# Kernel optimization log

Hardware: AMD Instinct MI355X
Metric: run time of the kernel (lower is better)

## Reference

```python
import jax, jax.numpy as jnp
import numpy as np

E, H2, V = 128, 512, 50000  # embedding_size, hidden_size*2, output_size
H4 = 2 * H2


def _gru_cell(x, h, W_ih, W_hh, b_ih, b_hh):
    # PyTorch GRU cell: gates ordered (r, z, n)
    gi = x @ W_ih.T + b_ih
    gh = h @ W_hh.T + b_hh
    i_r, i_z, i_n = jnp.split(gi, 3, axis=-1)
    h_r, h_z, h_n = jnp.split(gh, 3, axis=-1)
    r = jax.nn.sigmoid(i_r + h_r)
    z = jax.nn.sigmoid(i_z + h_z)
    n = jnp.tanh(i_n + r * h_n)
    return (1.0 - z) * n + z * h


def setup_inputs() -> dict:
    key = jax.random.key(0)
    ks = jax.random.split(key, 24)
    B, T = 64, 400
    s = 0.02
    inp = {
        "input_ids": jax.random.randint(ks[0], (B, 1), 0, V),
        "pre_hidden": jax.random.normal(ks[1], (2, B, H2), jnp.float32),
        "encoder_outputs": jax.random.normal(ks[2], (B, T, H2), jnp.float32),
        "source_input": jax.random.randint(ks[3], (B, T), 0, V),
        "coverage_vector": jax.random.uniform(ks[4], (B, 1, T), jnp.float32),
        "emb_table": jax.random.normal(ks[5], (V, E), jnp.float32) * s,
        "W_ih0": jax.random.normal(ks[6], (3 * H2, E), jnp.float32) * s,
        "W_hh0": jax.random.normal(ks[7], (3 * H2, H2), jnp.float32) * s,
        "b_ih0": jnp.zeros((3 * H2,), jnp.float32),
        "b_hh0": jnp.zeros((3 * H2,), jnp.float32),
        "W_ih1": jax.random.normal(ks[8], (3 * H2, H2), jnp.float32) * s,
        "W_hh1": jax.random.normal(ks[9], (3 * H2, H2), jnp.float32) * s,
        "b_ih1": jnp.zeros((3 * H2,), jnp.float32),
        "b_hh1": jnp.zeros((3 * H2,), jnp.float32),
        "align_W": jax.random.normal(ks[10], (1, 3 * H2), jnp.float32) * s,
        "align_b": jnp.zeros((1,), jnp.float32),
        "cov_W": jax.random.normal(ks[11], (H2, 1), jnp.float32) * s,
        "cov_b": jnp.zeros((H2,), jnp.float32),
        "fc1_W": jax.random.normal(ks[12], (H4, H4), jnp.float32) * s,
        "fc1_b": jnp.zeros((H4,), jnp.float32),
        "fc2_W": jax.random.normal(ks[13], (V, H4), jnp.float32) * s,
        "fc2_b": jnp.zeros((V,), jnp.float32),
        "gen_W": jax.random.normal(ks[14], (1, H4 + E), jnp.float32) * s,
        "gen_b": jnp.zeros((1,), jnp.float32),
    }
    return inp


def reference(input_ids, pre_hidden, encoder_outputs, source_input, coverage_vector,
              emb_table, W_ih0, W_hh0, b_ih0, b_hh0, W_ih1, W_hh1, b_ih1, b_hh1,
              align_W, align_b, cov_W, cov_b, fc1_W, fc1_b, fc2_W, fc2_b, gen_W, gen_b):
    B, T = source_input.shape
    # embedding lookup (dropout omitted / eval mode)
    emb = emb_table[input_ids[:, 0]]                          # [B,E]
    # 2-layer GRU, single decode step
    h0 = _gru_cell(emb, pre_hidden[0], W_ih0, W_hh0, b_ih0, b_hh0)
    h1 = _gru_cell(h0, pre_hidden[1], W_ih1, W_hh1, b_ih1, b_hh1)
    current_hidden = jnp.stack([h0, h1], axis=0)              # [2,B,H2]
    s = h1                                                    # [B,H2]
    cov = coverage_vector[:, 0, :]                            # [B,T]
    # coverage projection: Linear(1 -> H2)
    cov_feat = cov[:, :, None] * cov_W[:, 0][None, None, :] + cov_b  # [B,T,H2]
    s_rep = jnp.broadcast_to(s[:, None, :], (B, T, s.shape[-1]))
    combine = jnp.concatenate([encoder_outputs, s_rep, cov_feat], axis=-1)  # [B,T,3*H2]
    scores = jnp.einsum('bti,i->bt', combine, align_W[0]) + align_b[0]
    attn = jax.nn.softmax(jnp.tanh(scores), axis=1)           # [B,T]
    # coverage loss: sum of elementwise min(attn, coverage)
    coverage_loss = jnp.sum(jnp.minimum(attn, cov))
    new_coverage = coverage_vector + attn[:, None, :]         # [B,1,T]
    context = jnp.einsum('bt,bth->bh', attn, encoder_outputs) # [B,H2]
    ni = jnp.tanh(jnp.concatenate([s, context], axis=-1) @ fc1_W.T + fc1_b)
    logits = ni @ fc2_W.T + fc2_b                             # [B,V]
    Pvocab = jax.nn.softmax(logits, axis=1)
    # vectorized copy distribution: scatter-add attention mass onto source token ids
    batch_idx = jnp.arange(B)[:, None]
    copy_prob = jnp.zeros((B, logits.shape[1]), logits.dtype).at[batch_idx, source_input].add(attn)
    gen_in = jnp.concatenate([context, s, emb], axis=-1)      # [B,H4+E]
    p_gen = jax.nn.sigmoid(gen_in @ gen_W.T + gen_b)          # [B,1]
    out = Pvocab * p_gen + copy_prob * (1.0 - p_gen)
    return (out, current_hidden, attn[:, None, :], copy_prob, new_coverage, coverage_loss)
```

## Files before the change

### kernel.cpp

```cpp
#include <hip/hip_runtime.h>
#include <hip/hip_bf16.h>
#include <cstddef>

#define BB 64
#define TT 400
#define EE 128
#define HH 512
#define H4 1024
#define VV 50000
#define NCH 8
#define LSTR 136

#define OFF_OUT     0
#define OFF_CURHID  (BB*VV)
#define OFF_ATTN    (OFF_CURHID + 2*BB*HH)
#define OFF_COPY    (OFF_ATTN + BB*TT)
#define OFF_NEWCOV  (OFF_COPY + BB*VV)
#define OFF_LOSS    (OFF_NEWCOV + BB*TT)

#define WS_S      0
#define WS_ESC    (WS_S + BB*HH)
#define WS_ATTN   (WS_ESC + BB*TT)
#define WS_NIB    (WS_ATTN + BB*TT)
#define WS_A1     (WS_NIB + BB*H4/2)
#define WS_AX0    (WS_A1 + BB*H4/2)
#define WS_AH0    (WS_AX0 + BB*EE/2)
#define WS_AH1    (WS_AH0 + BB*HH/2)
#define WS_AX1    (WS_AH1 + BB*HH/2)
#define WS_PGEN   (WS_AX1 + BB*HH/2)
#define WS_RM     (WS_PGEN + 64)
#define WS_RS     (WS_RM + 64)
#define WS_CTXP   (WS_RS + 64)
#define WS_LOGITS (WS_CTXP + BB*NCH*HH)

typedef __attribute__((ext_vector_type(8))) short short8v;
typedef __attribute__((ext_vector_type(4))) short short4v;
typedef __attribute__((ext_vector_type(4))) float f32x4;

__device__ __forceinline__ float wredsum(float v) {
#pragma unroll
  for (int o = 32; o > 0; o >>= 1) v += __shfl_down(v, o, 64);
  return v;
}
__device__ __forceinline__ float wredmax(float v) {
#pragma unroll
  for (int o = 32; o > 0; o >>= 1) v = fmaxf(v, __shfl_down(v, o, 64));
  return v;
}
__device__ __forceinline__ float dot4(float4 a, float4 b) {
  return a.x*b.x + a.y*b.y + a.z*b.z + a.w*b.w;
}
__device__ __forceinline__ float sigmoidf(float x) { return 1.f / (1.f + expf(-x)); }
__device__ __forceinline__ short bfh(float f) {
  union { __hip_bfloat16 h; short s; } u; u.h = __float2bfloat16(f); return u.s;
}
__device__ __forceinline__ float bf2f(short s) {
  union { unsigned int u; float f; } v; v.u = ((unsigned int)(unsigned short)s) << 16; return v.f;
}

__global__ void zero_prep_kernel(float* __restrict__ p, float* __restrict__ loss,
                                 float* __restrict__ rs,
                                 const float* __restrict__ embt, const int* __restrict__ ids,
                                 const float* __restrict__ preh,
                                 const float* __restrict__ enc, const float* __restrict__ aW,
                                 short* __restrict__ ax0, short* __restrict__ ah0,
                                 short* __restrict__ ah1, float* __restrict__ esc) {
  int i = blockIdx.x * 256 + threadIdx.x;
  ((float4*)p)[i] = make_float4(0.f, 0.f, 0.f, 0.f);
  if (i == 0) loss[0] = 0.f;
  if (i < 64) rs[i] = 0.f;
  if (i < BB * EE) {
    int b = i >> 7, k = i & 127;
    ax0[i] = bfh(embt[(size_t)ids[b] * EE + k]);
  } else if (i < BB * EE + 2 * BB * HH) {
    int j = i - BB * EE;
    if (j < BB * HH) ah0[j] = bfh(preh[j]);
    else ah1[j - BB * HH] = bfh(preh[j]);
  }
  int wgid = blockIdx.x * 4 + (threadIdx.x >> 6);
  int lane = threadIdx.x & 63;
  int i8 = lane * 8;
  float4 a0 = *(const float4*)&aW[i8];
  float4 a1 = *(const float4*)&aW[i8 + 4];
  for (int idx = wgid; idx < BB * TT; idx += 12500) {
    const float* e = enc + (size_t)idx * HH + i8;
    float d = dot4(*(const float4*)&e[0], a0) + dot4(*(const float4*)&e[4], a1);
    d = wredsum(d);
    if (lane == 0) esc[idx] = d;
  }
}

template<int KX>
__global__ __launch_bounds__(768) void gru_mfma_kernel(
    const short* __restrict__ Ax, const short* __restrict__ Ah,
    const float* __restrict__ W_ih, const float* __restrict__ W_hh,
    const float* __restrict__ b_ih, const float* __restrict__ b_hh,
    const float* __restrict__ hprev,
    float* __restrict__ hout_f, float* __restrict__ hout_o,
    short* __restrict__ hout_b, int bstride) {
  __shared__ float Pf[12 * 256];
  const int w = threadIdx.x >> 6;
  const int lane = threadIdx.x & 63;
  const int r16 = lane & 15, kg = lane >> 4;
  const int j0 = (blockIdx.x & 31) * 16;
  const int bg = blockIdx.x >> 5;
  const int half = (w >= 6) ? 1 : 0;
  const int wv = w - half * 6;
  const int part = (wv >= 3) ? 1 : 0;
  const int g = wv - part * 3;
  const int K = part ? HH : KX;
  const int Kh = K >> 1;
  const float* Wm = part ? W_hh : W_ih;
  const short* Am = part ? Ah : Ax;

  f32x4 acc = {0.f, 0.f, 0.f, 0.f};
  const float* wp = Wm + (size_t)(g * HH + j0 + r16) * K + half * Kh + kg * 8;
  const short* ap = Am + (size_t)(bg * 16 + r16) * K + half * Kh + kg * 8;
#pragma unroll 4
  for (int k0 = 0; k0 < Kh; k0 += 32) {
    float4 w0 = *(const float4*)(wp + k0);
    float4 w1 = *(const float4*)(wp + k0 + 4);
    short8v a = *(const short8v*)(ap + k0);
    short8v bf;
    bf[0] = bfh(w0.x); bf[1] = bfh(w0.y); bf[2] = bfh(w0.z); bf[3] = bfh(w0.w);
    bf[4] = bfh(w1.x); bf[5] = bfh(w1.y); bf[6] = bfh(w1.z); bf[7] = bfh(w1.w);
    acc = __builtin_amdgcn_mfma_f32_16x16x32_bf16(a, bf, acc, 0, 0, 0);
  }
  float* pw = Pf + (half * 6 + part * 3 + g) * 256;
#pragma unroll
  for (int r = 0; r < 4; r++) pw[(kg * 4 + r) * 16 + r16] = acc[r];
  __syncthreads();
  if (w == 0) {
    int col = j0 + r16;
    float bir = b_ih[col] + b_hh[col];
    float biz = b_ih[HH + col] + b_hh[HH + col];
    float bin = b_ih[2 * HH + col], bhn = b_hh[2 * HH + col];
#pragma unroll
    for (int r = 0; r < 4; r++) {
      int m = kg * 4 + r;
      int row = bg * 16 + m;
      int o = m * 16 + r16;
      float ih_r = Pf[0 * 256 + o] + Pf[6 * 256 + o];
      float ih_z = Pf[1 * 256 + o] + Pf[7 * 256 + o];
      float ih_n = Pf[2 * 256 + o] + Pf[8 * 256 + o];
      float hh_r = Pf[3 * 256 + o] + Pf[9 * 256 + o];
      float hh_z = Pf[4 * 256 + o] + Pf[10 * 256 + o];
      float hh_n = Pf[5 * 256 + o] + Pf[11 * 256 + o];
      float rv = sigmoidf(ih_r + hh_r + bir);
      float zv = sigmoidf(ih_z + hh_z + biz);
      float nv = tanhf(ih_n + bin + rv * (hh_n + bhn));
      float h = (1.f - zv) * nv + zv * hprev[(size_t)row * HH + col];
      hout_f[(size_t)row * HH + col] = h;
      hout_o[(size_t)row * HH + col] = h;
      hout_b[(size_t)row * bstride + col] = bfh(h);
    }
  }
}

__global__ void attn_kernel(const float* __restrict__ esc, const float* __restrict__ cov,
                            const int* __restrict__ src, const float* __restrict__ s,
                            const float* __restrict__ aW, const float* __restrict__ ab,
                            const float* __restrict__ covW, const float* __restrict__ covb,
                            float* __restrict__ wattn, float* __restrict__ dout,
                            float* __restrict__ outc) {
  int b = blockIdx.x, tid = threadIdx.x;
  int lane = tid & 63, wid = tid >> 6;
  __shared__ float sred[24];
  __shared__ float bval[8];
  {
    float a2 = aW[2 * HH + tid];
    float p1 = s[(size_t)b * HH + tid] * aW[HH + tid];
    float p2 = covW[tid] * a2;
    float p3 = covb[tid] * a2;
    float r1 = wredsum(p1), r2 = wredsum(p2), r3 = wredsum(p3);
    if (lane == 0) { sred[wid] = r1; sred[8 + wid] = r2; sred[16 + wid] = r3; }
    __syncthreads();
    if (wid == 0) {
      float q1 = (lane < 8) ? sred[lane] : 0.f;      q1 = wredsum(q1);
      float q2 = (lane < 8) ? sred[8 + lane] : 0.f;  q2 = wredsum(q2);
      float q3 = (lane < 8) ? sred[16 + lane] : 0.f; q3 = wredsum(q3);
      if (lane == 0) { bval[2] = q1; bval[3] = q2; bval[4] = q3 + ab[0]; }
    }
    __syncthreads();
  }
  float sdot = bval[2], c1 = bval[3], c0 = bval[4];
  float cvt = (tid < TT) ? cov[b * TT + tid] : 0.f;
  float v = (tid < TT) ? tanhf(esc[b * TT + tid] + sdot + cvt * c1 + c0) : -1e30f;
  float wm = wredmax(v);
  if (lane == 0) sred[wid] = wm;
  __syncthreads();
  if (wid == 0) {
    float r = (lane < 8) ? sred[lane] : -1e30f;
    r = wredmax(r);
    if (lane == 0) bval[0] = r;
  }
  __syncthreads();
  float m = bval[0];
  float e = (tid < TT) ? expf(v - m) : 0.f;
  float wsm = wredsum(e);
  __syncthreads();
  if (lane == 0) sred[wid] = wsm;
  __syncthreads();
  if (wid == 0) {
    float r = (lane < 8) ? sred[lane] : 0.f;
    r = wredsum(r);
    if (lane == 0) bval[1] = r;
  }
  __syncthreads();
  float denom = bval[1];
  float a = e / denom;
  float lp = 0.f;
  if (tid < TT) {
    wattn[b * TT + tid] = a;
    dout[OFF_ATTN + b * TT + tid] = a;
    dout[OFF_NEWCOV + b * TT + tid] = cvt + a;
    lp = fminf(a, cvt);
    atomicAdd(&outc[(size_t)b * VV + src[b * TT + tid]], a);
  }
  float wl = wredsum(lp);
  __syncthreads();
  if (lane == 0) sred[wid] = wl;
  __syncthreads();
  if (wid == 0) {
    float r = (lane < 8) ? sred[lane] : 0.f;
    r = wredsum(r);
    if (lane == 0) atomicAdd(&dout[OFF_LOSS], r);
  }
}

__global__ void ctx_part_kernel(const float* __restrict__ enc, const float* __restrict__ attn,
                                float* __restrict__ ctxp) {
  int b = blockIdx.x, c = blockIdx.y;
  int h = threadIdx.x;
  __shared__ float as[TT / NCH];
  if (h < TT / NCH) as[h] = attn[b * TT + c * (TT / NCH) + h];
  __syncthreads();
  const float* e = enc + ((size_t)b * TT + c * (TT / NCH)) * HH + h;
  float acc = 0.f;
#pragma unroll 10
  for (int t = 0; t < TT / NCH; t++) acc += as[t] * e[(size_t)t * HH];
  ctxp[((size_t)b * NCH + c) * HH + h] = acc;
}

__global__ void ctxred_pgen_kernel(const float* __restrict__ ctxp, const float* __restrict__ s,
                                   const float* __restrict__ embt, const int* __restrict__ ids,
                                   const float* __restrict__ gW, const float* __restrict__ gb,
                                   short* __restrict__ a1, float* __restrict__ pgen) {
  int b = blockIdx.x, tid = threadIdx.x;
  int lane = tid & 63, wid = tid >> 6;
  __shared__ float sred[8];
  float acc = 0.f;
#pragma unroll
  for (int c = 0; c < NCH; c++) acc += ctxp[((size_t)b * NCH + c) * HH + tid];
  a1[(size_t)b * H4 + HH + tid] = bfh(acc);
  float part = acc * gW[tid] + s[b * HH + tid] * gW[HH + tid];
  if (tid < EE) part += embt[(size_t)ids[b] * EE + tid] * gW[2 * HH + tid];
  float w = wredsum(part);
  if (lane == 0) sred[wid] = w;
  __syncthreads();
  if (wid == 0) {
    float r = (lane < 8) ? sred[lane] : 0.f;
    r = wredsum(r);
    if (lane == 0) pgen[b] = sigmoidf(r + gb[0]);
  }
}

__global__ __launch_bounds__(256) void fc1_kernel(const short* __restrict__ a1,
                                                  const float* __restrict__ W,
                                                  const float* __restrict__ bias,
                                                  short* __restrict__ nib) {
  __shared__ float part[4096];
  const int w = threadIdx.x >> 6;
  const int lane = threadIdx.x & 63;
  const int r16 = lane & 15, kg = lane >> 4;
  const int v0 = blockIdx.x * 16;
  const int kb = w * 256;

  f32x4 acc0 = {0.f,0.f,0.f,0.f}, acc1 = {0.f,0.f,0.f,0.f};
  f32x4 acc2 = {0.f,0.f,0.f,0.f}, acc3 = {0.f,0.f,0.f,0.f};
  const float* wp = W + (size_t)(v0 + r16) * H4 + kb + kg * 8;
  const short* ap = a1 + (size_t)r16 * H4 + kb + kg * 8;
#pragma unroll 4
  for (int k0 = 0; k0 < 256; k0 += 32) {
    float4 w0 = *(const float4*)(wp + k0);
    float4 w1 = *(const float4*)(wp + k0 + 4);
    short8v a0 = *(const short8v*)(ap + k0);
    short8v a1v = *(const short8v*)(ap + 16 * H4 + k0);
    short8v a2 = *(const short8v*)(ap + 32 * H4 + k0);
    short8v a3 = *(const short8v*)(ap + 48 * H4 + k0);
    short8v bf;
    bf[0] = bfh(w0.x); bf[1] = bfh(w0.y); bf[2] = bfh(w0.z); bf[3] = bfh(w0.w);
    bf[4] = bfh(w1.x); bf[5] = bfh(w1.y); bf[6] = bfh(w1.z); bf[7] = bfh(w1.w);
    acc0 = __builtin_amdgcn_mfma_f32_16x16x32_bf16(a0, bf, acc0, 0, 0, 0);
    acc1 = __builtin_amdgcn_mfma_f32_16x16x32_bf16(a1v, bf, acc1, 0, 0, 0);
    acc2 = __builtin_amdgcn_mfma_f32_16x16x32_bf16(a2, bf, acc2, 0, 0, 0);
    acc3 = __builtin_amdgcn_mfma_f32_16x16x32_bf16(a3, bf, acc3, 0, 0, 0);
  }
  float* pb = part + w * 1024;
#pragma unroll
  for (int r = 0; r < 4; r++) {
    pb[(kg * 4 + r) * 16 + r16]      = acc0[r];
    pb[(16 + kg * 4 + r) * 16 + r16] = acc1[r];
    pb[(32 + kg * 4 + r) * 16 + r16] = acc2[r];
    pb[(48 + kg * 4 + r) * 16 + r16] = acc3[r];
  }
  __syncthreads();
  int idx = threadIdx.x * 4;
  int m = idx >> 4, c0 = idx & 15;
  f32x4 s0 = *(const f32x4*)(part + idx);
  f32x4 s1 = *(const f32x4*)(part + 1024 + idx);
  f32x4 s2 = *(const f32x4*)(part + 2048 + idx);
  f32x4 s3 = *(const f32x4*)(part + 3072 + idx);
  f32x4 bv = *(const f32x4*)(bias + v0 + c0);
  f32x4 o = s0 + s1 + s2 + s3 + bv;
#pragma unroll
  for (int j = 0; j < 4; j++)
    nib[(size_t)m * H4 + v0 + c0 + j] = bfh(tanhf(o[j]));
}

__global__ __launch_bounds__(256) void fc2_kernel(const short* __restrict__ nib,
                                                  const float* __restrict__ W,
                                                  const float* __restrict__ bias,
                                                  short* __restrict__ logits_bf,
                                                  float* __restrict__ rs) {
  __shared__ short Wl[64 * LSTR];
  __shared__ short Al[64 * LSTR];
  const int tid = threadIdx.x;
  const int w = tid >> 6, lane = tid & 63;
  const int r16 = lane & 15, kg = lane >> 4;
  const int v0 = blockIdx.x * 64;
  const int srow = tid >> 2, quad = tid & 3;
  const int vr = min(v0 + srow, VV - 1);

  f32x4 acc[4];
#pragma unroll
  for (int i = 0; i < 4; i++) acc[i] = (f32x4){0.f, 0.f, 0.f, 0.f};

  const float* wsrc = W + (size_t)vr * H4 + quad * 4;
  const short* asrc = nib + (size_t)srow * H4 + quad * 8;

  float4 wregA[8], wregB[8];
  short8v areg[4];
#pragma unroll
  for (int j = 0; j < 8; j++) wregA[j] = *(const float4*)(wsrc + j * 16);
#pragma unroll
  for (int j = 0; j < 8; j++) wregB[j] = *(const float4*)(wsrc + 128 + j * 16);
#pragma unroll
  for (int j = 0; j < 4; j++) areg[j] = *(const short8v*)(asrc + j * 32);

  auto step = [&](float4 (&wcur)[8], int ks) {
    char* dst = (char*)Wl + srow * (LSTR * 2) + quad * 8;
#pragma unroll
    for (int j = 0; j < 8; j++) {
      float4 f = wcur[j];
      short4v h; h[0] = bfh(f.x); h[1] = bfh(f.y); h[2] = bfh(f.z); h[3] = bfh(f.w);
      *(short4v*)(dst + j * 32) = h;
    }
    char* adst = (char*)Al + srow * (LSTR * 2) + quad * 16;
#pragma unroll
    for (int j = 0; j < 4; j++)
      *(short8v*)(adst + j * 64) = areg[j];
    __syncthreads();
    if (ks < 6) {
#pragma unroll
      for (int j = 0; j < 8; j++) wcur[j] = *(const float4*)(wsrc + (ks + 2) * 128 + j * 16);
    }
    if (ks < 7) {
#pragma unroll
      for (int j = 0; j < 4; j++) areg[j] = *(const short8v*)(asrc + (ks + 1) * 128 + j * 32);
    }
#pragma unroll
    for (int s = 0; s < 4; s++) {
      short8v wf = *(const short8v*)((char*)Wl + (w * 16 + r16) * (LSTR * 2) + s * 64 + kg * 16);
#pragma unroll
      for (int i = 0; i < 4; i++) {
        short8v af = *(const short8v*)((char*)Al + (i * 16 + r16) * (LSTR * 2) + s * 64 + kg * 16);
        acc[i] = __builtin_amdgcn_mfma_f32_16x16x32_bf16(af, wf, acc[i], 0, 0, 0);
      }
    }
    __syncthreads();
  };
#pragma unroll
  for (int it = 0; it < 4; it++) {
    step(wregA, 2 * it);
    step(wregB, 2 * it + 1);
  }

  float* sc = (float*)Wl;
#pragma unroll
  for (int i = 0; i < 4; i++)
#pragma unroll
    for (int r = 0; r < 4; r++)
      sc[(i * 16 + kg * 4 + r) * 64 + w * 16 + r16] = acc[i][r];
  __syncthreads();
  int m = tid >> 2, q = tid & 3;
  int colbase = v0 + q * 16;
  float esum = 0.f;
  if (colbase < VV) {
    const float* scp = sc + m * 64 + q * 16;
    short8v lo, hi;
#pragma unroll
    for (int j = 0; j < 8; j++) {
      short lb = bfh(scp[j] + bias[colbase + j]);
      lo[j] = lb;
      esum += expf(bf2f(lb));
    }
#pragma unroll
    for (int j = 0; j < 8; j++) {
      short lb = bfh(scp[8 + j] + bias[colbase + 8 + j]);
      hi[j] = lb;
      esum += expf(bf2f(lb));
    }
    *(short8v*)(logits_bf + (size_t)m * VV + colbase)     = lo;
    *(short8v*)(logits_bf + (size_t)m * VV + colbase + 8) = hi;
  }
  esum += __shfl_down(esum, 2, 4);
  esum += __shfl_down(esum, 1, 4);
  if (q == 0) atomicAdd(&rs[m], esum);
}

__global__ void final_kernel(const short* __restrict__ logits_bf, const float* __restrict__ rs,
                             const float* __restrict__ pgen,
                             const float* __restrict__ copy, float* __restrict__ out) {
  int i = blockIdx.x * 256 + threadIdx.x;
  int b = (i * 4) / VV;
  float p = pgen[b], s = rs[b];
  short4v l = ((const short4v*)logits_bf)[i];
  float4 c = ((const float4*)copy)[i];
  float q = 1.f - p;
  float ps = p / s;
  float4 o;
  o.x = expf(bf2f(l[0])) * ps + c.x * q;
  o.y = expf(bf2f(l[1])) * ps + c.y * q;
  o.z = expf(bf2f(l[2])) * ps + c.z * q;
  o.w = expf(bf2f(l[3])) * ps + c.w * q;
  ((float4*)out)[i] = o;
}

extern "C" void kernel_launch(void* const* d_in, const int* in_sizes, int n_in,
                              void* d_out, int out_size, void* d_ws, size_t ws_size,
                              hipStream_t stream) {
  const int*   ids  = (const int*)d_in[0];
  const float* preh = (const float*)d_in[1];
  const float* enc  = (const float*)d_in[2];
  const int*   src  = (const int*)d_in[3];
  const float* cov  = (const float*)d_in[4];
  const float* embt = (const float*)d_in[5];
  const float* Wih0 = (const float*)d_in[6];
  const float* Whh0 = (const float*)d_in[7];
  const float* bih0 = (const float*)d_in[8];
  const float* bhh0 = (const float*)d_in[9];
  const float* Wih1 = (const float*)d_in[10];
  const float* Whh1 = (const float*)d_in[11];
  const float* bih1 = (const float*)d_in[12];
  const float* bhh1 = (const float*)d_in[13];
  const float* aW   = (const float*)d_in[14];
  const float* ab   = (const float*)d_in[15];
  const float* covW = (const float*)d_in[16];
  const float* covb = (const float*)d_in[17];
  const float* f1W  = (const float*)d_in[18];
  const float* f1b  = (const float*)d_in[19];
  const float* f2W  = (const float*)d_in[20];
  const float* f2b  = (const float*)d_in[21];
  const float* gW   = (const float*)d_in[22];
  const float* gb   = (const float*)d_in[23];
  float* out = (float*)d_out;
  float* ws  = (float*)d_ws;

  zero_prep_kernel<<<3125, 256, 0, stream>>>(out + OFF_COPY, out + OFF_LOSS, ws + WS_RS,
                                             embt, ids, preh, enc, aW,
                                             (short*)(ws + WS_AX0), (short*)(ws + WS_AH0),
                                             (short*)(ws + WS_AH1), ws + WS_ESC);
  gru_mfma_kernel<EE><<<128, 768, 0, stream>>>(
      (const short*)(ws + WS_AX0), (const short*)(ws + WS_AH0),
      Wih0, Whh0, bih0, bhh0, preh,
      out + OFF_CURHID, out + OFF_CURHID, (short*)(ws + WS_AX1), HH);
  gru_mfma_kernel<HH><<<128, 768, 0, stream>>>(
      (const short*)(ws + WS_AX1), (const short*)(ws + WS_AH1),
      Wih1, Whh1, bih1, bhh1, preh + BB * HH,
      ws + WS_S, out + OFF_CURHID + BB * HH, (short*)(ws + WS_A1), H4);
  attn_kernel<<<64, 512, 0, stream>>>(ws + WS_ESC, cov, src, ws + WS_S,
                                      aW, ab, covW, covb,
                                      ws + WS_ATTN, out, out + OFF_COPY);
  ctx_part_kernel<<<dim3(64, NCH), 512, 0, stream>>>(enc, ws + WS_ATTN, ws + WS_CTXP);
  ctxred_pgen_kernel<<<64, 512, 0, stream>>>(ws + WS_CTXP, ws + WS_S, embt, ids, gW, gb,
                                             (short*)(ws + WS_A1), ws + WS_PGEN);
  fc1_kernel<<<64, 256, 0, stream>>>((const short*)(ws + WS_A1), f1W, f1b,
                                     (short*)(ws + WS_NIB));
  fc2_kernel<<<782, 256, 0, stream>>>((const short*)(ws + WS_NIB), f2W, f2b,
                                      (short*)(ws + WS_LOGITS), ws + WS_RS);
  final_kernel<<<3125, 256, 0, stream>>>((const short*)(ws + WS_LOGITS), ws + WS_RS,
                                         ws + WS_PGEN, out + OFF_COPY, out);
}
```

Before: 122.4 us.

## Fuse attention softmax into context kernel and read fc2 activations from global

Merges the attention softmax kernel with the context partial-sum kernel. Each of the 8 chunk blocks per batch row recomputes the full softmax redundantly, and only chunk 0 writes the attention outputs, coverage, copy scatter and loss. This removes one launch and the workspace round-trip for the attention weights. Separately, fc2 no longer stages the bf16 activation tile in shared memory and loads MFMA A-fragments directly from global/L2 memory. That halves the LDS footprint but adds repeated global loads inside the inner loop.

```diff
diff --git a/kernel.cpp b/kernel.cpp
--- a/kernel.cpp
+++ b/kernel.cpp
@@ -9,6 +9,7 @@
 #define H4 1024
 #define VV 50000
 #define NCH 8
+#define TCH (TT/NCH)
 #define LSTR 136
 
 #define OFF_OUT     0
@@ -20,8 +21,7 @@
 
 #define WS_S      0
 #define WS_ESC    (WS_S + BB*HH)
-#define WS_ATTN   (WS_ESC + BB*TT)
-#define WS_NIB    (WS_ATTN + BB*TT)
+#define WS_NIB    (WS_ESC + BB*TT)
 #define WS_A1     (WS_NIB + BB*H4/2)
 #define WS_AX0    (WS_A1 + BB*H4/2)
 #define WS_AH0    (WS_AX0 + BB*EE/2)
@@ -157,14 +157,17 @@
   }
 }
 
-__global__ void attn_kernel(const float* __restrict__ esc, const float* __restrict__ cov,
-                            const int* __restrict__ src, const float* __restrict__ s,
-                            const float* __restrict__ aW, const float* __restrict__ ab,
-                            const float* __restrict__ covW, const float* __restrict__ covb,
-                            float* __restrict__ wattn, float* __restrict__ dout,
-                            float* __restrict__ outc) {
-  int b = blockIdx.x, tid = threadIdx.x;
+__global__ __launch_bounds__(512) void attn_ctx_kernel(
+    const float* __restrict__ esc, const float* __restrict__ cov,
+    const int* __restrict__ src, const float* __restrict__ s,
+    const float* __restrict__ aW, const float* __restrict__ ab,
+    const float* __restrict__ covW, const float* __restrict__ covb,
+    const float* __restrict__ enc,
+    float* __restrict__ dout, float* __restrict__ outc, float* __restrict__ ctxp) {
+  int b = blockIdx.x, c = blockIdx.y;
+  int tid = threadIdx.x;
   int lane = tid & 63, wid = tid >> 6;
+  __shared__ float as[TT];
   __shared__ float sred[24];
   __shared__ float bval[8];
   {
@@ -209,37 +212,32 @@
   __syncthreads();
   float denom = bval[1];
   float a = e / denom;
-  float lp = 0.f;
-  if (tid < TT) {
-    wattn[b * TT + tid] = a;
-    dout[OFF_ATTN + b * TT + tid] = a;
-    dout[OFF_NEWCOV + b * TT + tid] = cvt + a;
-    lp = fminf(a, cvt);
-    atomicAdd(&outc[(size_t)b * VV + src[b * TT + tid]], a);
-  }
-  float wl = wredsum(lp);
-  __syncthreads();
-  if (lane == 0) sred[wid] = wl;
-  __syncthreads();
-  if (wid == 0) {
-    float r = (lane < 8) ? sred[lane] : 0.f;
-    r = wredsum(r);
-    if (lane == 0) atomicAdd(&dout[OFF_LOSS], r);
-  }
-}
-
-__global__ void ctx_part_kernel(const float* __restrict__ enc, const float* __restrict__ attn,
-                                float* __restrict__ ctxp) {
-  int b = blockIdx.x, c = blockIdx.y;
-  int h = threadIdx.x;
-  __shared__ float as[TT / NCH];
-  if (h < TT / NCH) as[h] = attn[b * TT + c * (TT / NCH) + h];
-  __syncthreads();
-  const float* e = enc + ((size_t)b * TT + c * (TT / NCH)) * HH + h;
+  if (tid < TT) as[tid] = a;
+  if (c == 0) {
+    float lp = 0.f;
+    if (tid < TT) {
+      dout[OFF_ATTN + b * TT + tid] = a;
+      dout[OFF_NEWCOV + b * TT + tid] = cvt + a;
+      lp = fminf(a, cvt);
+      atomicAdd(&outc[(size_t)b * VV + src[b * TT + tid]], a);
+    }
+    float wl = wredsum(lp);
+    __syncthreads();
+    if (lane == 0) sred[wid] = wl;
+    __syncthreads();
+    if (wid == 0) {
+      float r = (lane < 8) ? sred[lane] : 0.f;
+      r = wredsum(r);
+      if (lane == 0) atomicAdd(&dout[OFF_LOSS], r);
+    }
+  }
+  __syncthreads();
+  const float* ep = enc + ((size_t)b * TT + c * TCH) * HH + tid;
+  const float* ac = as + c * TCH;
   float acc = 0.f;
 #pragma unroll 10
-  for (int t = 0; t < TT / NCH; t++) acc += as[t] * e[(size_t)t * HH];
-  ctxp[((size_t)b * NCH + c) * HH + h] = acc;
+  for (int t = 0; t < TCH; t++) acc += ac[t] * ep[(size_t)t * HH];
+  ctxp[((size_t)b * NCH + c) * HH + tid] = acc;
 }
 
 __global__ void ctxred_pgen_kernel(const float* __restrict__ ctxp, const float* __restrict__ s,
@@ -324,7 +322,6 @@
                                                   short* __restrict__ logits_bf,
                                                   float* __restrict__ rs) {
   __shared__ short Wl[64 * LSTR];
-  __shared__ short Al[64 * LSTR];
   const int tid = threadIdx.x;
   const int w = tid >> 6, lane = tid & 63;
   const int r16 = lane & 15, kg = lane >> 4;
@@ -337,16 +334,13 @@
   for (int i = 0; i < 4; i++) acc[i] = (f32x4){0.f, 0.f, 0.f, 0.f};
 
   const float* wsrc = W + (size_t)vr * H4 + quad * 4;
-  const short* asrc = nib + (size_t)srow * H4 + quad * 8;
+  const short* abase = nib + (size_t)r16 * H4 + kg * 8;
 
   float4 wregA[8], wregB[8];
-  short8v areg[4];
 #pragma unroll
   for (int j = 0; j < 8; j++) wregA[j] = *(const float4*)(wsrc + j * 16);
 #pragma unroll
   for (int j = 0; j < 8; j++) wregB[j] = *(const float4*)(wsrc + 128 + j * 16);
-#pragma unroll
-  for (int j = 0; j < 4; j++) areg[j] = *(const short8v*)(asrc + j * 32);
 
   auto step = [&](float4 (&wcur)[8], int ks) {
     char* dst = (char*)Wl + srow * (LSTR * 2) + quad * 8;
@@ -356,25 +350,18 @@
       short4v h; h[0] = bfh(f.x); h[1] = bfh(f.y); h[2] = bfh(f.z); h[3] = bfh(f.w);
       *(short4v*)(dst + j * 32) = h;
     }
-    char* adst = (char*)Al + srow * (LSTR * 2) + quad * 16;
-#pragma unroll
-    for (int j = 0; j < 4; j++)
-      *(short8v*)(adst + j * 64) = areg[j];
     __syncthreads();
     if (ks < 6) {
 #pragma unroll
       for (int j = 0; j < 8; j++) wcur[j] = *(const float4*)(wsrc + (ks + 2) * 128 + j * 16);
     }
-    if (ks < 7) {
-#pragma unroll
-      for (int j = 0; j < 4; j++) areg[j] = *(const short8v*)(asrc + (ks + 1) * 128 + j * 32);
-    }
+    const short* ak = abase + ks * 128;
 #pragma unroll
     for (int s = 0; s < 4; s++) {
       short8v wf = *(const short8v*)((char*)Wl + (w * 16 + r16) * (LSTR * 2) + s * 64 + kg * 16);
 #pragma unroll
       for (int i = 0; i < 4; i++) {
-        short8v af = *(const short8v*)((char*)Al + (i * 16 + r16) * (LSTR * 2) + s * 64 + kg * 16);
+        short8v af = *(const short8v*)(ak + (size_t)i * 16 * H4 + s * 32);
         acc[i] = __builtin_amdgcn_mfma_f32_16x16x32_bf16(af, wf, acc[i], 0, 0, 0);
       }
     }
@@ -479,10 +466,9 @@
       (const short*)(ws + WS_AX1), (const short*)(ws + WS_AH1),
       Wih1, Whh1, bih1, bhh1, preh + BB * HH,
       ws + WS_S, out + OFF_CURHID + BB * HH, (short*)(ws + WS_A1), H4);
-  attn_kernel<<<64, 512, 0, stream>>>(ws + WS_ESC, cov, src, ws + WS_S,
-                                      aW, ab, covW, covb,
-                                      ws + WS_ATTN, out, out + OFF_COPY);
-  ctx_part_kernel<<<dim3(64, NCH), 512, 0, stream>>>(enc, ws + WS_ATTN, ws + WS_CTXP);
+  attn_ctx_kernel<<<dim3(64, NCH), 512, 0, stream>>>(
+      ws + WS_ESC, cov, src, ws + WS_S, aW, ab, covW, covb, enc,
+      out, out + OFF_COPY, ws + WS_CTXP);
   ctxred_pgen_kernel<<<64, 512, 0, stream>>>(ws + WS_CTXP, ws + WS_S, embt, ids, gW, gb,
                                              (short*)(ws + WS_A1), ws + WS_PGEN);
   fc1_kernel<<<64, 256, 0, stream>>>((const short*)(ws + WS_A1), f1W, f1b,
```

After: 155.4 us. 27.0% more time.
